# Kernel optimization log

Measured on AMD Instinct MI355X. Metric: run time of the kernel, lower is better.

The kernel has to match this reference:

```python
import jax, jax.numpy as jnp
import numpy as np
from jax import lax

EPS = 1e-05
Q = 4          # window size (hard-coded in BotBlock)
HEADS = 4
DIM = 16       # bottleneck(64) // heads(4)


def conv3x3(x, w, b):
    # x: [N,C,H,W], w: [O,I,3,3]
    y = lax.conv_general_dilated(x, w, (1, 1), ((1, 1), (1, 1)),
                                 dimension_numbers=('NCHW', 'OIHW', 'NCHW'))
    return y + b[None, :, None, None]


def batchnorm(x, gamma, beta):
    # training-mode BN: batch statistics over (N,H,W), biased variance
    m = jnp.mean(x, axis=(0, 2, 3), keepdims=True)
    v = jnp.var(x, axis=(0, 2, 3), keepdims=True)
    xn = (x - m) * lax.rsqrt(v + EPS)
    return xn * gamma[None, :, None, None] + beta[None, :, None, None]


def rel_to_abs(x):
    # x: [B, H, L, 2L-1] -> [B, H, L, L] via pad/reshape trick
    B, H, L, _ = x.shape
    x = jnp.pad(x, ((0, 0), (0, 0), (0, 0), (0, 1)))          # [B,H,L,2L]
    flat = x.reshape(B, H, -1)                                  # [B,H,2L*L]
    flat = jnp.pad(flat, ((0, 0), (0, 0), (0, L - 1)))
    final = flat.reshape(B, H, L + 1, 2 * L - 1)
    return final[:, :, :L, L - 1:]                              # [B,H,L,L]


def relative_logits_1d(q, rel_k, perm):
    # q: [b, n, h, w, d], rel_k: [2w-1, d]
    b, n, h, w, d = q.shape
    rl = jnp.einsum('bnhwd,md->bnhwm', q, rel_k)
    rl = rl.reshape(b, n * h, w, 2 * w - 1)
    rl = rel_to_abs(rl)                                         # [b, n*h, w, w]
    rl = rl.reshape(b, n, h, w, w)
    rl = jnp.broadcast_to(rl[:, :, :, None], (b, n, h, h, w, w))
    return jnp.transpose(rl, perm)


def rel_pos_attention(q, k, v, rel_w, rel_h):
    # q,k,v: [b, heads, h, w, d]
    b, n, h, w, d = q.shape
    q = q * (d ** -0.5)
    logits = jnp.einsum('bnhwd,bnpqd->bnhwpq', q, k)
    logits = logits + relative_logits_1d(q, rel_w, (0, 1, 2, 4, 3, 5))
    logits = logits + relative_logits_1d(jnp.transpose(q, (0, 1, 3, 2, 4)),
                                         rel_h, (0, 1, 4, 2, 5, 3))
    weights = jax.nn.softmax(logits.reshape(b, n, h, w, h * w), axis=-1)
    weights = weights.reshape(b, n, h, w, h, w)
    out = jnp.einsum('bnhwpq,bnpqd->bhwnd', weights, v)         # [b,h,w,n,d]
    return out.reshape(b, h, w, n * d)                          # fold heads


def setup_inputs() -> dict:
    key = jax.random.key(0)
    ks = jax.random.split(key, 16)
    C_in, C_bot, C_out = 64, 64, 256
    inp = {
        'x': jax.random.normal(ks[0], (2, C_in, 256, 256), jnp.float32),
        'conv1_w': jax.random.normal(ks[1], (C_bot, C_in, 3, 3), jnp.float32) * 0.05,
        'conv1_b': jnp.zeros((C_bot,), jnp.float32),
        'bn1_g': jnp.ones((C_bot,), jnp.float32),
        'bn1_b': jnp.zeros((C_bot,), jnp.float32),
        'wq': jax.random.normal(ks[2], (C_bot, HEADS, DIM), jnp.float32) * 0.01,
        'wk': jax.random.normal(ks[3], (C_bot, HEADS, DIM), jnp.float32) * 0.01,
        'wv': jax.random.normal(ks[4], (C_bot, HEADS, DIM), jnp.float32) * 0.01,
        'rel_w': jax.random.normal(ks[5], (2 * Q - 1, DIM), jnp.float32) * (DIM ** -0.5),
        'rel_h': jax.random.normal(ks[6], (2 * Q - 1, DIM), jnp.float32) * (DIM ** -0.5),
        'bn2_g': jnp.ones((C_bot,), jnp.float32),
        'bn2_b': jnp.zeros((C_bot,), jnp.float32),
        'conv3_w': jax.random.normal(ks[7], (C_out, C_bot, 3, 3), jnp.float32) * 0.05,
        'conv3_b': jnp.zeros((C_out,), jnp.float32),
        # NOTE: original init_zero=True zeros bn3 gamma; we randomize it so the
        # output (and gradients) are non-trivial for kernel correctness checks.
        'bn3_g': jax.random.normal(ks[8], (C_out,), jnp.float32),
        'bn3_b': jnp.zeros((C_out,), jnp.float32),
    }
    return inp


def reference(x, conv1_w, conv1_b, bn1_g, bn1_b, wq, wk, wv, rel_w, rel_h,
              bn2_g, bn2_b, conv3_w, conv3_b, bn3_g, bn3_b):
    N, C, H, W = x.shape
    P_h, P_w = H // Q, W // Q
    # raw memory reinterpretation into 4x4 blocks (matches torch .reshape)
    xb = x.reshape(N * P_h * P_w, C, Q, Q)
    out = jax.nn.relu(batchnorm(conv3x3(xb, conv1_w, conv1_b), bn1_g, bn1_b))
    # GroupPointWise projections: NCHW -> NHWC then einsum
    feat = jnp.transpose(out, (0, 2, 3, 1))                     # [b,h,w,c]
    q = jnp.einsum('bhwc,cnp->bnhwp', feat, wq)
    k = jnp.einsum('bhwc,cnp->bnhwp', feat, wk)
    v = jnp.einsum('bhwc,cnp->bnhwp', feat, wv)
    o = rel_pos_attention(q, k, v, rel_w, rel_h)                # [b,h,w,c]
    o = jnp.transpose(o, (0, 3, 1, 2))                          # NCHW
    o = jax.nn.relu(batchnorm(o, bn2_g, bn2_b))
    o = batchnorm(conv3x3(o, conv3_w, conv3_b), bn3_g, bn3_b)   # no act
    C1 = o.shape[1]
    o = o.reshape(N, C1, H, W)
    return jax.nn.relu(o)
```

## Files before the change

### kernel.cpp

```cpp
#include <hip/hip_runtime.h>
#include <stdint.h>


#define EPSV 1e-5f
#define INV_N (1.0f / 131072.0f)

typedef unsigned short u16;
typedef __attribute__((ext_vector_type(8))) short short8b;
typedef __attribute__((ext_vector_type(4))) float f32x4;

__device__ __forceinline__ u16 f2bf(float f) {
  unsigned u = __float_as_uint(f);
  u += 0x7fffu + ((u >> 16) & 1u);
  return (u16)(u >> 16);
}
__device__ __forceinline__ float bf2f(u16 h) {
  return __uint_as_float((unsigned)h << 16);
}

__device__ __forceinline__ float bn_scale(const float* __restrict__ acc,
                                          const float* __restrict__ gam,
                                          const float* __restrict__ bet,
                                          int C, int c, float& shift) {
  float S = acc[c], S2 = acc[C + c];
  float mean = S * INV_N;
  float var  = S2 * INV_N - mean * mean;
  float rstd = rsqrtf(var + EPSV);
  float sc = gam[c] * rstd;
  shift = bet[c] - mean * sc;
  return sc;
}

__global__ __launch_bounds__(256) void prep_kernel(const float* __restrict__ w1,
                                                   const float* __restrict__ w3,
                                                   const float* __restrict__ wq,
                                                   const float* __restrict__ wk,
                                                   const float* __restrict__ wv,
                                                   u16* __restrict__ wp1,
                                                   u16* __restrict__ wp3,
                                                   u16* __restrict__ wqkvT) {
  int i = blockIdx.x * 256 + threadIdx.x;
  const int tot1 = 18 * 64 * 40;
  const int tot3 = 9 * 256 * 64;
  if (i < tot1) {
    int ch = i / (64 * 40); int r = i - ch * 64 * 40; int o = r / 40; int kk = r - o * 40;
    float v = 0.f;
    if (kk < 32) { int k = ch * 32 + kk; int tap = k >> 6; int c = k & 63;
                   v = w1[o * 576 + c * 9 + tap]; }
    wp1[i] = f2bf(v);
  } else if (i < tot1 + tot3) {
    int j = i - tot1;
    int tap = j >> 14; int r = j & 16383; int o = r >> 6; int c = r & 63;
    wp3[j] = f2bf(w3[o * 576 + c * 9 + tap]);
  } else if (i < tot1 + tot3 + 192 * 64) {
    int j = i - tot1 - tot3;
    int oc = j >> 6, c = j & 63;
    const float* src = (oc < 64) ? wq : (oc < 128) ? wk : wv;
    wqkvT[j] = f2bf(src[(c << 6) + (oc & 63)]);
  }
}

__global__ __launch_bounds__(256) void conv1_kernel(const float* __restrict__ x,
                                                    const u16* __restrict__ wp,
                                                    u16* __restrict__ bufb,
                                                    float* __restrict__ partials1) {
  __shared__ __align__(16) char featA[257 * 128];
  __shared__ __align__(16) char ldsW[2][64 * 80];
  const int t = threadIdx.x;
  const int lane = t & 63, w = t >> 6;
  const int lrow = lane & 15, lk = lane >> 4;
  const int wm = w >> 1, wn = w & 1;
  const size_t Mbase = (size_t)blockIdx.x * 256;

  int rel[9];
  {
    const int pi = lrow >> 2, pj = lrow & 3;
#pragma unroll
    for (int tap = 0; tap < 9; ++tap) {
      const int ti = tap / 3, tj = tap - ti * 3;
      int si = pi + ti - 1, sj = pj + tj - 1;
      bool valid = ((unsigned)si < 4u) && ((unsigned)sj < 4u);
      rel[tap] = valid ? ((si * 4 + sj) << 7) : (1 << 24);
    }
  }

#pragma unroll
  for (int i = 0; i < 16; ++i) {
    float4 v = *reinterpret_cast<const float4*>(x + Mbase * 64 + i * 1024 + t * 4);
    const int c = t >> 2, p0 = (t & 3) * 4;
    float vv[4] = {v.x, v.y, v.z, v.w};
#pragma unroll
    for (int j = 0; j < 4; ++j) {
      int row = i * 16 + p0 + j;
      int byte = row * 128 + ((((c >> 3) ^ (row & 7)) << 4) | ((c & 7) << 1));
      *reinterpret_cast<u16*>(featA + byte) = f2bf(vv[j]);
    }
  }
  if (t < 8) *reinterpret_cast<uint4*>(featA + 256 * 128 + t * 16) = uint4{0, 0, 0, 0};

  uint4 s0, s1;
  {
    const u16* sp = wp;
    s0 = *reinterpret_cast<const uint4*>(sp + (size_t)t * 8);
    if (t < 64) s1 = *reinterpret_cast<const uint4*>(sp + (size_t)(t + 256) * 8);
    *reinterpret_cast<uint4*>(ldsW[0] + t * 16) = s0;
    if (t < 64) *reinterpret_cast<uint4*>(ldsW[0] + (t + 256) * 16) = s1;
  }
  __syncthreads();

  f32x4 acc[8][2] = {};
#pragma unroll
  for (int chn = 0; chn < 18; ++chn) {
    const int cur = chn & 1;
    const int tap = chn >> 1, kk = chn & 1;
    if (chn + 1 < 18) {
      const u16* sp = wp + (chn + 1) * 2560;
      s0 = *reinterpret_cast<const uint4*>(sp + (size_t)t * 8);
      if (t < 64) s1 = *reinterpret_cast<const uint4*>(sp + (size_t)(t + 256) * 8);
    }
    const int kkg = (kk << 6) | (lk << 4);
    short8b bw[2];
#pragma unroll
    for (int n = 0; n < 2; ++n)
      bw[n] = *reinterpret_cast<const short8b*>(ldsW[cur] + (wn * 32 + n * 16 + lrow) * 80 + lk * 16);
#pragma unroll
    for (int m = 0; m < 8; ++m) {
      int ad = ((wm * 128 + m * 16) << 7) + rel[tap];
      ad = ad < 32768 ? ad : 32768;
      ad += (kkg ^ ((ad >> 3) & 0x70));
      short8b af = *reinterpret_cast<const short8b*>(featA + ad);
#pragma unroll
      for (int n = 0; n < 2; ++n)
        acc[m][n] = __builtin_amdgcn_mfma_f32_16x16x32_bf16(af, bw[n], acc[m][n], 0, 0, 0);
    }
    if (chn + 1 < 18) {
      *reinterpret_cast<uint4*>(ldsW[cur ^ 1] + t * 16) = s0;
      if (t < 64) *reinterpret_cast<uint4*>(ldsW[cur ^ 1] + (t + 256) * 16) = s1;
    }
    __syncthreads();
  }

#pragma unroll
  for (int m = 0; m < 8; ++m) {
    const size_t rowg0 = Mbase + wm * 128 + m * 16 + lk * 4;
#pragma unroll
    for (int n = 0; n < 2; ++n) {
      const int o = wn * 32 + n * 16 + lrow;
#pragma unroll
      for (int r = 0; r < 4; ++r)
        bufb[(rowg0 + r) * 64 + o] = f2bf(acc[m][n][r]);
    }
  }

  float* pst = reinterpret_cast<float*>(featA);
  if (t < 128) pst[t] = 0.f;
  __syncthreads();
#pragma unroll
  for (int n = 0; n < 2; ++n) {
    float s = 0.f, s2 = 0.f;
#pragma unroll
    for (int m = 0; m < 8; ++m)
#pragma unroll
      for (int r = 0; r < 4; ++r) {
        float v = acc[m][n][r];
        s += v; s2 = fmaf(v, v, s2);
      }
    s += __shfl_xor(s, 16); s2 += __shfl_xor(s2, 16);
    s += __shfl_xor(s, 32); s2 += __shfl_xor(s2, 32);
    if (lk == 0) {
      const int o = wn * 32 + n * 16 + lrow;
      atomicAdd(&pst[o], s);
      atomicAdd(&pst[64 + o], s2);
    }
  }
  __syncthreads();
  if (t < 128) partials1[(size_t)blockIdx.x * 128 + t] = pst[t];
}

__global__ __launch_bounds__(256) void reduce12_kernel(const float* __restrict__ p,
                                                       float* __restrict__ acc, int nrows) {
  const int c = blockIdx.x, t = threadIdx.x;
  float s = 0.f;
  for (int i = t; i < nrows; i += 256) s += p[(size_t)i * 128 + c];
#pragma unroll
  for (int off = 32; off > 0; off >>= 1) s += __shfl_down(s, off);
  __shared__ float red[4];
  if ((t & 63) == 0) red[t >> 6] = s;
  __syncthreads();
  if (t == 0) acc[c] = red[0] + red[1] + red[2] + red[3];
}

__global__ __launch_bounds__(256) void attn_kernel(u16* __restrict__ buf,
                                                   const u16* __restrict__ wqkvT,
                                                   const float* __restrict__ relw,
                                                   const float* __restrict__ relh,
                                                   const float* __restrict__ acc1,
                                                   const float* __restrict__ g1,
                                                   const float* __restrict__ b1,
                                                   float* __restrict__ partials2) {
  __shared__ float scsh[64][2];
  __shared__ float pstA[128];
  __shared__ __align__(16) u16 feat_l[4][1024];
  __shared__ __align__(16) float qkvf[4][3264];
  const int t = threadIdx.x, u = t >> 6, lane = t & 63;
  const size_t b = (size_t)blockIdx.x * 4 + u;
  float* Wf = qkvf[u];

  if (t < 64) {
    float sh; float sc = bn_scale(acc1, g1, b1, 64, t, sh);
    scsh[t][0] = sc; scsh[t][1] = sh;
  }
  if (t < 128) pstA[t] = 0.f;
  __syncthreads();

  {
    const int pos = lane >> 2, cq = lane & 3;
    const u16* src = buf + b * 1024 + pos * 64 + cq * 16;
    short8b v0 = *reinterpret_cast<const short8b*>(src);
    short8b v1 = *reinterpret_cast<const short8b*>(src + 8);
    short8b p0, p1;
#pragma unroll
    for (int j = 0; j < 8; ++j) {
      const int c0 = cq * 16 + j, c1 = cq * 16 + 8 + j;
      p0[j] = (short)f2bf(fmaxf(fmaf(bf2f((u16)v0[j]), scsh[c0][0], scsh[c0][1]), 0.f));
      p1[j] = (short)f2bf(fmaxf(fmaf(bf2f((u16)v1[j]), scsh[c1][0], scsh[c1][1]), 0.f));
    }
    const int g0 = (cq * 2) ^ (pos & 7), g1g = (cq * 2 + 1) ^ (pos & 7);
    *reinterpret_cast<short8b*>(&feat_l[u][pos * 64 + g0 * 8]) = p0;
    *reinterpret_cast<short8b*>(&feat_l[u][pos * 64 + g1g * 8]) = p1;
  }

  const int dq = lane & 15, lk = lane >> 4;
  short8b afr[2];
#pragma unroll
  for (int ch = 0; ch < 2; ++ch) {
    const int kg = ch * 4 + lk;
    afr[ch] = *reinterpret_cast<const short8b*>(&feat_l[u][dq * 64 + ((kg ^ (dq & 7)) * 8)]);
  }
#pragma unroll
  for (int ct = 0; ct < 12; ++ct) {
    f32x4 d = {0.f, 0.f, 0.f, 0.f};
#pragma unroll
    for (int ch = 0; ch < 2; ++ch) {
      short8b bfr = *reinterpret_cast<const short8b*>(&wqkvT[(ct * 16 + dq) * 64 + ch * 32 + lk * 8]);
      d = __builtin_amdgcn_mfma_f32_16x16x32_bf16(afr[ch], bfr, d, 0, 0, 0);
    }
    if (ct < 4) {
      float* dst = Wf + ct * 280;
#pragma unroll
      for (int r = 0; r < 4; ++r) dst[(lk * 4 + r) * 17 + dq] = d[r] * 0.25f;
    } else {
      float* dst = (ct < 8) ? (Wf + 1120 + (ct - 4) * 264) : (Wf + 2176 + (ct - 8) * 264);
      const int cp = dq ^ (lk << 2);
#pragma unroll
      for (int r = 0; r < 4; ++r) dst[(lk * 4 + r) * 16 + cp] = d[r];
    }
  }

  const int n = lk, qp = dq;
  const int qi = qp >> 2, qj = qp & 3;
  float q_[16];
  {
    const float* qb = Wf + n * 280 + qp * 17;
#pragma unroll
    for (int d2 = 0; d2 < 16; ++d2) q_[d2] = qb[d2];
  }
  float rwq[4], rhq[4];
  {
    const float* rwp = relw + (3 - qj) * 16;
    const float* rhp = relh + (3 - qi) * 16;
#pragma unroll
    for (int m = 0; m < 4; ++m) {
      float a1 = 0.f, a2 = 0.f;
#pragma unroll
      for (int d2 = 0; d2 < 16; ++d2) {
        a1 = fmaf(q_[d2], rwp[m * 16 + d2], a1);
        a2 = fmaf(q_[d2], rhp[m * 16 + d2], a2);
      }
      rwq[m] = a1; rhq[m] = a2;
    }
  }
  float lo[16]; float mx = -1e30f;
  const float* kbase = Wf + 1120 + n * 264;
#pragma unroll
  for (int kp = 0; kp < 16; ++kp) {
    const float4* kr = reinterpret_cast<const float4*>(kbase + kp * 16);
    float s = rwq[kp & 3] + rhq[kp >> 2];
#pragma unroll
    for (int g = 0; g < 4; ++g) {
      float4 kv = kr[g];
      const int lg = (g ^ (kp >> 2)) * 4;
      s = fmaf(q_[lg], kv.x, s); s = fmaf(q_[lg + 1], kv.y, s);
      s = fmaf(q_[lg + 2], kv.z, s); s = fmaf(q_[lg + 3], kv.w, s);
    }
    lo[kp] = s; mx = fmaxf(mx, s);
  }
  float ssum = 0.f;
#pragma unroll
  for (int kp = 0; kp < 16; ++kp) { float e = __expf(lo[kp] - mx); lo[kp] = e; ssum += e; }
  const float inv = 1.0f / ssum;
  float ov[16];
#pragma unroll
  for (int j = 0; j < 16; ++j) ov[j] = 0.f;
  const float* vbase = Wf + 2176 + n * 264;
#pragma unroll
  for (int kp = 0; kp < 16; ++kp) {
    const float4* vr = reinterpret_cast<const float4*>(vbase + kp * 16);
    const float wgt = lo[kp];
#pragma unroll
    for (int g = 0; g < 4; ++g) {
      float4 vv = vr[g];
      const int lg = (g ^ (kp >> 2)) * 4;
      ov[lg] = fmaf(wgt, vv.x, ov[lg]);
      ov[lg + 1] = fmaf(wgt, vv.y, ov[lg + 1]);
      ov[lg + 2] = fmaf(wgt, vv.z, ov[lg + 2]);
      ov[lg + 3] = fmaf(wgt, vv.w, ov[lg + 3]);
    }
  }
#pragma unroll
  for (int j = 0; j < 16; ++j) ov[j] *= inv;

  {
    short8b o0, o1;
#pragma unroll
    for (int j = 0; j < 8; ++j) {
      o0[j] = (short)f2bf(ov[j]);
      o1[j] = (short)f2bf(ov[8 + j]);
    }
    u16* dstb = buf + b * 1024 + qp * 64 + (n << 4);
    *reinterpret_cast<short8b*>(dstb) = o0;
    *reinterpret_cast<short8b*>(dstb + 8) = o1;
  }

  {
    float* fl = Wf;
#pragma unroll
    for (int j = 0; j < 16; ++j) fl[qp * 69 + n * 16 + j] = ov[j];
    const int c = lane;
    float s = 0.f, s2 = 0.f;
#pragma unroll
    for (int pos = 0; pos < 16; ++pos) {
      float v = fl[pos * 69 + c];
      s += v; s2 = fmaf(v, v, s2);
    }
    atomicAdd(&pstA[c], s);
    atomicAdd(&pstA[64 + c], s2);
  }
  __syncthreads();
  if (t < 128) partials2[(size_t)blockIdx.x * 128 + t] = pstA[t];
}

__global__ __launch_bounds__(256, 2) void conv3_kernel(const u16* __restrict__ src,
                                                       const u16* __restrict__ wp,
                                                       const float* __restrict__ acc2,
                                                       const float* __restrict__ g2,
                                                       const float* __restrict__ b2,
                                                       u16* __restrict__ y3b,
                                                       float* __restrict__ partials3) {
  __shared__ __align__(16) u16 featB[257 * 64];
  __shared__ __align__(16) u16 ldsW[2][128 * 64];
  __shared__ float scsh[128];
  const int t = threadIdx.x;
  const int lane = t & 63, w = t >> 6;
  const int lrow = lane & 15, lk = lane >> 4;
  const int wm = w >> 1, wn = w & 1;
  const int Nbase = blockIdx.x * 256;
  const int ohalf = blockIdx.y;

  int rel[9];
  {
    const int pi = lrow >> 2, pj = lrow & 3;
#pragma unroll
    for (int tap = 0; tap < 9; ++tap) {
      const int ti = tap / 3, tj = tap - ti * 3;
      int si = pi + ti - 1, sj = pj + tj - 1;
      bool valid = ((unsigned)si < 4u) && ((unsigned)sj < 4u);
      rel[tap] = valid ? ((si * 4 + sj) << 7) : (1 << 24);
    }
  }

  if (t < 64) {
    float sh; float sc = bn_scale(acc2, g2, b2, 64, t, sh);
    scsh[t * 2] = sc; scsh[t * 2 + 1] = sh;
  }

  const int so = t >> 1, shalf = t & 1, so7 = so & 7;
  {
    const u16* wsrc = wp + ohalf * 8192 + so * 64 + shalf * 32;
    uint4 w0 = *reinterpret_cast<const uint4*>(wsrc);
    uint4 w1 = *reinterpret_cast<const uint4*>(wsrc + 8);
    uint4 w2 = *reinterpret_cast<const uint4*>(wsrc + 16);
    uint4 w3v = *reinterpret_cast<const uint4*>(wsrc + 24);
    char* dst = (char*)ldsW[0] + so * 128;
    const int gb = shalf * 4;
    *reinterpret_cast<uint4*>(dst + (((gb + 0) ^ so7) << 4)) = w0;
    *reinterpret_cast<uint4*>(dst + (((gb + 1) ^ so7) << 4)) = w1;
    *reinterpret_cast<uint4*>(dst + (((gb + 2) ^ so7) << 4)) = w2;
    *reinterpret_cast<uint4*>(dst + (((gb + 3) ^ so7) << 4)) = w3v;
  }
  __syncthreads();

  {
    const u16* srow = src + (size_t)(Nbase + t) * 64;
    char* drow = (char*)featB + t * 128;
    const int r7 = t & 7;
#pragma unroll
    for (int g = 0; g < 8; ++g) {
      short8b v = *reinterpret_cast<const short8b*>(srow + g * 8);
      short8b pk;
#pragma unroll
      for (int j = 0; j < 8; ++j) {
        const int c = g * 8 + j;
        pk[j] = (short)f2bf(fmaxf(fmaf(bf2f((u16)v[j]), scsh[c * 2], scsh[c * 2 + 1]), 0.f));
      }
      *reinterpret_cast<short8b*>(drow + ((g ^ r7) << 4)) = pk;
    }
  }
  if (t < 8) *reinterpret_cast<uint4*>((char*)featB + 32768 + t * 16) = uint4{0, 0, 0, 0};

  uint4 r0, r1, r2, r3v;
  {
    const u16* wsrc = wp + 16384 + ohalf * 8192 + so * 64 + shalf * 32;
    r0 = *reinterpret_cast<const uint4*>(wsrc);
    r1 = *reinterpret_cast<const uint4*>(wsrc + 8);
    r2 = *reinterpret_cast<const uint4*>(wsrc + 16);
    r3v = *reinterpret_cast<const uint4*>(wsrc + 24);
  }
  __syncthreads();

  f32x4 acc[4][8] = {};
  const char* fB = (const char*)featB;
  const int swzA0 = (lk << 4) ^ ((lrow & 7) << 4);
  const int swzA1 = (64 | (lk << 4)) ^ ((lrow & 7) << 4);

#pragma unroll
  for (int tap = 0; tap < 9; ++tap) {
    const int cur = tap & 1;
    const char* lW = (const char*)ldsW[cur];
    short8b aw0[4], aw1[4];
#pragma unroll
    for (int m = 0; m < 4; ++m) {
      const int rowoff = (wm * 64 + m * 16 + lrow) << 7;
      aw0[m] = *reinterpret_cast<const short8b*>(lW + rowoff + swzA0);
      aw1[m] = *reinterpret_cast<const short8b*>(lW + rowoff + swzA1);
    }
#pragma unroll
    for (int n = 0; n < 8; ++n) {
      int ad0 = ((wn * 128 + n * 16) << 7) + rel[tap];
      ad0 = ad0 < 32768 ? ad0 : 32768;
      const int swz = (ad0 >> 3) & 0x70;
      short8b bf0 = *reinterpret_cast<const short8b*>(fB + ad0 + ((lk << 4) ^ swz));
      short8b bf1 = *reinterpret_cast<const short8b*>(fB + ad0 + ((64 | (lk << 4)) ^ swz));
#pragma unroll
      for (int m = 0; m < 4; ++m) {
        acc[m][n] = __builtin_amdgcn_mfma_f32_16x16x32_bf16(aw0[m], bf0, acc[m][n], 0, 0, 0);
        acc[m][n] = __builtin_amdgcn_mfma_f32_16x16x32_bf16(aw1[m], bf1, acc[m][n], 0, 0, 0);
      }
    }
    if (tap < 8) {
      char* dst = (char*)ldsW[cur ^ 1] + so * 128;
      const int gb = shalf * 4;
      *reinterpret_cast<uint4*>(dst + (((gb + 0) ^ so7) << 4)) = r0;
      *reinterpret_cast<uint4*>(dst + (((gb + 1) ^ so7) << 4)) = r1;
      *reinterpret_cast<uint4*>(dst + (((gb + 2) ^ so7) << 4)) = r2;
      *reinterpret_cast<uint4*>(dst + (((gb + 3) ^ so7) << 4)) = r3v;
      if (tap < 7) {
        const u16* wsrc = wp + (tap + 2) * 16384 + ohalf * 8192 + so * 64 + shalf * 32;
        r0 = *reinterpret_cast<const uint4*>(wsrc);
        r1 = *reinterpret_cast<const uint4*>(wsrc + 8);
        r2 = *reinterpret_cast<const uint4*>(wsrc + 16);
        r3v = *reinterpret_cast<const uint4*>(wsrc + 24);
      }
    }
    __syncthreads();
  }

#pragma unroll
  for (int m = 0; m < 4; ++m) {
    const int o = ohalf * 128 + wm * 64 + m * 16 + lk * 4;
#pragma unroll
    for (int n = 0; n < 8; ++n) {
      const int colg = Nbase + wn * 128 + n * 16 + lrow;
      const int b = colg >> 4, p = colg & 15;
      u16* dst = y3b + (size_t)b * 4096 + (size_t)o * 16 + p;
#pragma unroll
      for (int r = 0; r < 4; ++r)
        dst[r * 16] = f2bf(acc[m][n][r]);
    }
  }

  float* pst = reinterpret_cast<float*>(featB);
  pst[t] = 0.f;
  __syncthreads();
#pragma unroll
  for (int m = 0; m < 4; ++m) {
#pragma unroll
    for (int r = 0; r < 4; ++r) {
      float s = 0.f, s2 = 0.f;
#pragma unroll
      for (int n = 0; n < 8; ++n) {
        float v = acc[m][n][r];
        s += v; s2 = fmaf(v, v, s2);
      }
      s += __shfl_xor(s, 1); s2 += __shfl_xor(s2, 1);
      s += __shfl_xor(s, 2); s2 += __shfl_xor(s2, 2);
      s += __shfl_xor(s, 4); s2 += __shfl_xor(s2, 4);
      s += __shfl_xor(s, 8); s2 += __shfl_xor(s2, 8);
      if (lrow == 0) {
        const int ch = wm * 64 + m * 16 + lk * 4 + r;
        atomicAdd(&pst[ch], s);
        atomicAdd(&pst[128 + ch], s2);
      }
    }
  }
  __syncthreads();
  partials3[((size_t)(ohalf * 512 + blockIdx.x)) * 256 + t] = pst[t];
}

__global__ __launch_bounds__(256) void reduce3_kernel(const float* __restrict__ p,
                                                      float* __restrict__ acc3) {
  const int c2 = blockIdx.x, t = threadIdx.x;
  const int kind = c2 >> 8, c = c2 & 255;
  const int h = c >> 7, chl = c & 127;
  float s = 0.f;
  for (int i = t; i < 512; i += 256)
    s += p[((size_t)(h * 512 + i)) * 256 + kind * 128 + chl];
#pragma unroll
  for (int off = 32; off > 0; off >>= 1) s += __shfl_down(s, off);
  __shared__ float red[4];
  if ((t & 63) == 0) red[t >> 6] = s;
  __syncthreads();
  if (t == 0) acc3[kind * 256 + c] = red[0] + red[1] + red[2] + red[3];
}

__global__ __launch_bounds__(256) void final_kernel(const u16* __restrict__ y3b,
                                                    float* __restrict__ out,
                                                    const float* __restrict__ acc3,
                                                    const float* __restrict__ g3,
                                                    const float* __restrict__ b3) {
  const size_t i = ((size_t)blockIdx.x * 256 + threadIdx.x) * 8;
  const int c = (int)((i >> 4) & 255);
  float sh; const float sc = bn_scale(acc3, g3, b3, 256, c, sh);
  short8b v = *reinterpret_cast<const short8b*>(y3b + i);
  float4 o0, o1;
  o0.x = fmaxf(fmaf(bf2f((u16)v[0]), sc, sh), 0.f);
  o0.y = fmaxf(fmaf(bf2f((u16)v[1]), sc, sh), 0.f);
  o0.z = fmaxf(fmaf(bf2f((u16)v[2]), sc, sh), 0.f);
  o0.w = fmaxf(fmaf(bf2f((u16)v[3]), sc, sh), 0.f);
  o1.x = fmaxf(fmaf(bf2f((u16)v[4]), sc, sh), 0.f);
  o1.y = fmaxf(fmaf(bf2f((u16)v[5]), sc, sh), 0.f);
  o1.z = fmaxf(fmaf(bf2f((u16)v[6]), sc, sh), 0.f);
  o1.w = fmaxf(fmaf(bf2f((u16)v[7]), sc, sh), 0.f);
  *reinterpret_cast<float4*>(out + i) = o0;
  *reinterpret_cast<float4*>(out + i + 4) = o1;
}

extern "C" void kernel_launch(void* const* d_in, const int* in_sizes, int n_in,
                              void* d_out, int out_size, void* d_ws, size_t ws_size,
                              hipStream_t stream) {
  const float* x   = (const float*)d_in[0];
  const float* w1  = (const float*)d_in[1];
  const float* g1  = (const float*)d_in[3];
  const float* bb1 = (const float*)d_in[4];
  const float* wq  = (const float*)d_in[5];
  const float* wk  = (const float*)d_in[6];
  const float* wv  = (const float*)d_in[7];
  const float* rw  = (const float*)d_in[8];
  const float* rh  = (const float*)d_in[9];
  const float* g2  = (const float*)d_in[10];
  const float* bb2 = (const float*)d_in[11];
  const float* w3  = (const float*)d_in[12];
  const float* g3  = (const float*)d_in[14];
  const float* bb3 = (const float*)d_in[15];
  float* out = (float*)d_out;
  float* ws  = (float*)d_ws;

  u16*   bufb   = (u16*)ws;
  u16*   y3b    = bufb + 8388608;
  u16*   wp1    = y3b + 33554432;
  u16*   wp3    = wp1 + 46080;
  u16*   wqkvT  = wp3 + 147456;
  float* acc1   = ws + 21074432;
  float* acc2   = acc1 + 128;
  float* acc3   = acc2 + 128;
  float* part1  = acc3 + 512;
  float* part2  = part1 + 65536;
  float* part3  = part2 + 262144;

  prep_kernel<<<804, 256, 0, stream>>>(w1, w3, wq, wk, wv, wp1, wp3, wqkvT);
  conv1_kernel<<<512, 256, 0, stream>>>(x, wp1, bufb, part1);
  reduce12_kernel<<<128, 256, 0, stream>>>(part1, acc1, 512);
  attn_kernel<<<2048, 256, 0, stream>>>(bufb, wqkvT, rw, rh, acc1, g1, bb1, part2);
  reduce12_kernel<<<128, 256, 0, stream>>>(part2, acc2, 2048);
  conv3_kernel<<<dim3(512, 2), 256, 0, stream>>>(bufb, wp3, acc2, g2, bb2, y3b, part3);
  reduce3_kernel<<<512, 256, 0, stream>>>(part3, acc3);
  final_kernel<<<16384, 256, 0, stream>>>(y3b, out, acc3, g3, bb3);
}
```

Measured before the change: 163.9 us.

## Fold relative-position logits into QKV MFMA and use packed bf16 conversions

```diff
diff --git a/kernel.cpp b/kernel.cpp
--- a/kernel.cpp
+++ b/kernel.cpp
@@ -16,6 +16,11 @@
 }
 __device__ __forceinline__ float bf2f(u16 h) {
   return __uint_as_float((unsigned)h << 16);
+}
+__device__ __forceinline__ unsigned cvtpk(float lo, float hi) {
+  unsigned r;
+  asm("v_cvt_pk_bf16_f32 %0, %1, %2" : "=v"(r) : "v"(lo), "v"(hi));
+  return r;
 }
 
 __device__ __forceinline__ float bn_scale(const float* __restrict__ acc,
@@ -36,6 +41,8 @@
                                                    const float* __restrict__ wq,
                                                    const float* __restrict__ wk,
                                                    const float* __restrict__ wv,
+                                                   const float* __restrict__ relw,
+                                                   const float* __restrict__ relh,
                                                    u16* __restrict__ wp1,
                                                    u16* __restrict__ wp3,
                                                    u16* __restrict__ wqkvT) {
@@ -57,6 +64,17 @@
     int oc = j >> 6, c = j & 63;
     const float* src = (oc < 64) ? wq : (oc < 128) ? wk : wv;
     wqkvT[j] = f2bf(src[(c << 6) + (oc & 63)]);
+  } else if (i < tot1 + tot3 + 192 * 64 + 4096) {
+    int j = i - tot1 - tot3 - 192 * 64;
+    int c = j & 63; int col = (j >> 6) & 31; int tbl = j >> 11;
+    int n = col >> 3, m = col & 7;
+    float v = 0.f;
+    if (m < 7) {
+      const float* rel = tbl ? relh : relw;
+#pragma unroll
+      for (int d = 0; d < 16; ++d) v += wq[c * 64 + n * 16 + d] * rel[m * 16 + d];
+    }
+    wqkvT[(192 + tbl * 32 + col) * 64 + c] = f2bf(v);
   }
 }
 
@@ -84,16 +102,21 @@
     }
   }
 
-#pragma unroll
-  for (int i = 0; i < 16; ++i) {
-    float4 v = *reinterpret_cast<const float4*>(x + Mbase * 64 + i * 1024 + t * 4);
-    const int c = t >> 2, p0 = (t & 3) * 4;
-    float vv[4] = {v.x, v.y, v.z, v.w};
-#pragma unroll
-    for (int j = 0; j < 4; ++j) {
-      int row = i * 16 + p0 + j;
-      int byte = row * 128 + ((((c >> 3) ^ (row & 7)) << 4) | ((c & 7) << 1));
-      *reinterpret_cast<u16*>(featA + byte) = f2bf(vv[j]);
+  {
+    const int cp = t >> 3, ph = t & 7;
+    const int gsw = ((cp >> 2) << 4) | ((cp & 3) << 2);
+#pragma unroll
+    for (int i = 0; i < 16; ++i) {
+      const float* bp = x + Mbase * 64 + i * 1024 + cp * 32 + ph * 2;
+      float2 a = *reinterpret_cast<const float2*>(bp);
+      float2 b = *reinterpret_cast<const float2*>(bp + 16);
+#pragma unroll
+      for (int j = 0; j < 2; ++j) {
+        const int row = i * 16 + ph * 2 + j;
+        unsigned pk = cvtpk(j ? a.y : a.x, j ? b.y : b.x);
+        const int byte = row * 128 + (gsw ^ ((row & 7) << 4));
+        *reinterpret_cast<unsigned*>(featA + byte) = pk;
+      }
     }
   }
   if (t < 8) *reinterpret_cast<uint4*>(featA + 256 * 128 + t * 16) = uint4{0, 0, 0, 0};
@@ -192,8 +215,6 @@
 
 __global__ __launch_bounds__(256) void attn_kernel(u16* __restrict__ buf,
                                                    const u16* __restrict__ wqkvT,
-                                                   const float* __restrict__ relw,
-                                                   const float* __restrict__ relh,
                                                    const float* __restrict__ acc1,
                                                    const float* __restrict__ g1,
                                                    const float* __restrict__ b1,
@@ -201,10 +222,12 @@
   __shared__ float scsh[64][2];
   __shared__ float pstA[128];
   __shared__ __align__(16) u16 feat_l[4][1024];
-  __shared__ __align__(16) float qkvf[4][3264];
+  __shared__ __align__(16) float qkvf[4][3200];
+  __shared__ __align__(16) float relLs[4][1152];
   const int t = threadIdx.x, u = t >> 6, lane = t & 63;
   const size_t b = (size_t)blockIdx.x * 4 + u;
   float* Wf = qkvf[u];
+  float* rL = relLs[u];
 
   if (t < 64) {
     float sh; float sc = bn_scale(acc1, g1, b1, 64, t, sh);
@@ -218,16 +241,18 @@
     const u16* src = buf + b * 1024 + pos * 64 + cq * 16;
     short8b v0 = *reinterpret_cast<const short8b*>(src);
     short8b v1 = *reinterpret_cast<const short8b*>(src + 8);
-    short8b p0, p1;
+    float f[16];
 #pragma unroll
     for (int j = 0; j < 8; ++j) {
       const int c0 = cq * 16 + j, c1 = cq * 16 + 8 + j;
-      p0[j] = (short)f2bf(fmaxf(fmaf(bf2f((u16)v0[j]), scsh[c0][0], scsh[c0][1]), 0.f));
-      p1[j] = (short)f2bf(fmaxf(fmaf(bf2f((u16)v1[j]), scsh[c1][0], scsh[c1][1]), 0.f));
-    }
+      f[j]     = fmaxf(fmaf(bf2f((u16)v0[j]), scsh[c0][0], scsh[c0][1]), 0.f);
+      f[8 + j] = fmaxf(fmaf(bf2f((u16)v1[j]), scsh[c1][0], scsh[c1][1]), 0.f);
+    }
+    uint4 q0{cvtpk(f[0], f[1]), cvtpk(f[2], f[3]), cvtpk(f[4], f[5]), cvtpk(f[6], f[7])};
+    uint4 q1{cvtpk(f[8], f[9]), cvtpk(f[10], f[11]), cvtpk(f[12], f[13]), cvtpk(f[14], f[15])};
     const int g0 = (cq * 2) ^ (pos & 7), g1g = (cq * 2 + 1) ^ (pos & 7);
-    *reinterpret_cast<short8b*>(&feat_l[u][pos * 64 + g0 * 8]) = p0;
-    *reinterpret_cast<short8b*>(&feat_l[u][pos * 64 + g1g * 8]) = p1;
+    *reinterpret_cast<uint4*>(&feat_l[u][pos * 64 + g0 * 8]) = q0;
+    *reinterpret_cast<uint4*>(&feat_l[u][pos * 64 + g1g * 8]) = q1;
   }
 
   const int dq = lane & 15, lk = lane >> 4;
@@ -238,7 +263,7 @@
     afr[ch] = *reinterpret_cast<const short8b*>(&feat_l[u][dq * 64 + ((kg ^ (dq & 7)) * 8)]);
   }
 #pragma unroll
-  for (int ct = 0; ct < 12; ++ct) {
+  for (int ct = 0; ct < 16; ++ct) {
     f32x4 d = {0.f, 0.f, 0.f, 0.f};
 #pragma unroll
     for (int ch = 0; ch < 2; ++ch) {
@@ -246,14 +271,20 @@
       d = __builtin_amdgcn_mfma_f32_16x16x32_bf16(afr[ch], bfr, d, 0, 0, 0);
     }
     if (ct < 4) {
-      float* dst = Wf + ct * 280;
+      float* dst = Wf + ct * 272;
 #pragma unroll
       for (int r = 0; r < 4; ++r) dst[(lk * 4 + r) * 17 + dq] = d[r] * 0.25f;
+    } else if (ct < 12) {
+      float* dst = (ct < 8) ? (Wf + 1088 + (ct - 4) * 264) : (Wf + 2144 + (ct - 8) * 264);
+      const int cp = dq ^ (lk << 2);
+#pragma unroll
+      for (int r = 0; r < 4; ++r) dst[(lk * 4 + r) * 16 + cp] = d[r];
     } else {
-      float* dst = (ct < 8) ? (Wf + 1120 + (ct - 4) * 264) : (Wf + 2176 + (ct - 8) * 264);
-      const int cp = dq ^ (lk << 2);
-#pragma unroll
-      for (int r = 0; r < 4; ++r) dst[(lk * 4 + r) * 16 + cp] = d[r];
+      const int rc = ct - 12, tbl = rc >> 1;
+      const int nn = ((rc & 1) << 1) | (dq >> 3), mm = dq & 7;
+      float* dst = rL + tbl * 576 + nn * 144 + mm;
+#pragma unroll
+      for (int r = 0; r < 4; ++r) dst[(lk * 4 + r) * 9] = d[r] * 0.25f;
     }
   }
 
@@ -261,27 +292,19 @@
   const int qi = qp >> 2, qj = qp & 3;
   float q_[16];
   {
-    const float* qb = Wf + n * 280 + qp * 17;
+    const float* qb = Wf + n * 272 + qp * 17;
 #pragma unroll
     for (int d2 = 0; d2 < 16; ++d2) q_[d2] = qb[d2];
   }
   float rwq[4], rhq[4];
   {
-    const float* rwp = relw + (3 - qj) * 16;
-    const float* rhp = relh + (3 - qi) * 16;
-#pragma unroll
-    for (int m = 0; m < 4; ++m) {
-      float a1 = 0.f, a2 = 0.f;
-#pragma unroll
-      for (int d2 = 0; d2 < 16; ++d2) {
-        a1 = fmaf(q_[d2], rwp[m * 16 + d2], a1);
-        a2 = fmaf(q_[d2], rhp[m * 16 + d2], a2);
-      }
-      rwq[m] = a1; rhq[m] = a2;
-    }
+    const float* rw = rL + n * 144 + qp * 9 + (3 - qj);
+    const float* rh = rL + 576 + n * 144 + qp * 9 + (3 - qi);
+#pragma unroll
+    for (int k = 0; k < 4; ++k) { rwq[k] = rw[k]; rhq[k] = rh[k]; }
   }
   float lo[16]; float mx = -1e30f;
-  const float* kbase = Wf + 1120 + n * 264;
+  const float* kbase = Wf + 1088 + n * 264;
 #pragma unroll
   for (int kp = 0; kp < 16; ++kp) {
     const float4* kr = reinterpret_cast<const float4*>(kbase + kp * 16);
@@ -302,7 +325,7 @@
   float ov[16];
 #pragma unroll
   for (int j = 0; j < 16; ++j) ov[j] = 0.f;
-  const float* vbase = Wf + 2176 + n * 264;
+  const float* vbase = Wf + 2144 + n * 264;
 #pragma unroll
   for (int kp = 0; kp < 16; ++kp) {
     const float4* vr = reinterpret_cast<const float4*>(vbase + kp * 16);
@@ -321,15 +344,11 @@
   for (int j = 0; j < 16; ++j) ov[j] *= inv;
 
   {
-    short8b o0, o1;
-#pragma unroll
-    for (int j = 0; j < 8; ++j) {
-      o0[j] = (short)f2bf(ov[j]);
-      o1[j] = (short)f2bf(ov[8 + j]);
-    }
+    uint4 o0{cvtpk(ov[0], ov[1]), cvtpk(ov[2], ov[3]), cvtpk(ov[4], ov[5]), cvtpk(ov[6], ov[7])};
+    uint4 o1{cvtpk(ov[8], ov[9]), cvtpk(ov[10], ov[11]), cvtpk(ov[12], ov[13]), cvtpk(ov[14], ov[15])};
     u16* dstb = buf + b * 1024 + qp * 64 + (n << 4);
-    *reinterpret_cast<short8b*>(dstb) = o0;
-    *reinterpret_cast<short8b*>(dstb + 8) = o1;
+    *reinterpret_cast<uint4*>(dstb) = o0;
+    *reinterpret_cast<uint4*>(dstb + 8) = o1;
   }
 
   {
@@ -378,12 +397,10 @@
       rel[tap] = valid ? ((si * 4 + sj) << 7) : (1 << 24);
     }
   }
-
   if (t < 64) {
     float sh; float sc = bn_scale(acc2, g2, b2, 64, t, sh);
     scsh[t * 2] = sc; scsh[t * 2 + 1] = sh;
   }
-
   const int so = t >> 1, shalf = t & 1, so7 = so & 7;
   {
     const u16* wsrc = wp + ohalf * 8192 + so * 64 + shalf * 32;
@@ -399,7 +416,6 @@
     *reinterpret_cast<uint4*>(dst + (((gb + 3) ^ so7) << 4)) = w3v;
   }
   __syncthreads();
-
   {
     const u16* srow = src + (size_t)(Nbase + t) * 64;
     char* drow = (char*)featB + t * 128;
@@ -407,17 +423,17 @@
 #pragma unroll
     for (int g = 0; g < 8; ++g) {
       short8b v = *reinterpret_cast<const short8b*>(srow + g * 8);
-      short8b pk;
+      float f[8];
 #pragma unroll
       for (int j = 0; j < 8; ++j) {
         const int c = g * 8 + j;
-        pk[j] = (short)f2bf(fmaxf(fmaf(bf2f((u16)v[j]), scsh[c * 2], scsh[c * 2 + 1]), 0.f));
+        f[j] = fmaxf(fmaf(bf2f((u16)v[j]), scsh[c * 2], scsh[c * 2 + 1]), 0.f);
       }
-      *reinterpret_cast<short8b*>(drow + ((g ^ r7) << 4)) = pk;
+      uint4 pk{cvtpk(f[0], f[1]), cvtpk(f[2], f[3]), cvtpk(f[4], f[5]), cvtpk(f[6], f[7])};
+      *reinterpret_cast<uint4*>(drow + ((g ^ r7) << 4)) = pk;
     }
   }
   if (t < 8) *reinterpret_cast<uint4*>((char*)featB + 32768 + t * 16) = uint4{0, 0, 0, 0};
-
   uint4 r0, r1, r2, r3v;
   {
     const u16* wsrc = wp + 16384 + ohalf * 8192 + so * 64 + shalf * 32;
@@ -427,12 +443,10 @@
     r3v = *reinterpret_cast<const uint4*>(wsrc + 24);
   }
   __syncthreads();
-
   f32x4 acc[4][8] = {};
   const char* fB = (const char*)featB;
   const int swzA0 = (lk << 4) ^ ((lrow & 7) << 4);
   const int swzA1 = (64 | (lk << 4)) ^ ((lrow & 7) << 4);
-
 #pragma unroll
   for (int tap = 0; tap < 9; ++tap) {
     const int cur = tap & 1;
@@ -474,7 +488,6 @@
     }
     __syncthreads();
   }
-
 #pragma unroll
   for (int m = 0; m < 4; ++m) {
     const int o = ohalf * 128 + wm * 64 + m * 16 + lk * 4;
@@ -484,11 +497,9 @@
       const int b = colg >> 4, p = colg & 15;
       u16* dst = y3b + (size_t)b * 4096 + (size_t)o * 16 + p;
 #pragma unroll
-      for (int r = 0; r < 4; ++r)
-        dst[r * 16] = f2bf(acc[m][n][r]);
-    }
-  }
-
+      for (int r = 0; r < 4; ++r) dst[r * 16] = f2bf(acc[m][n][r]);
+    }
+  }
   float* pst = reinterpret_cast<float*>(featB);
   pst[t] = 0.f;
   __syncthreads();
@@ -576,23 +587,23 @@
   float* ws  = (float*)d_ws;
 
   u16*   bufb   = (u16*)ws;
-  u16*   y3b    = bufb + 8388608;
-  u16*   wp1    = y3b + 33554432;
+  u16*   y3     = bufb + 8388608;
+  u16*   wp1    = y3 + 33554432;
   u16*   wp3    = wp1 + 46080;
   u16*   wqkvT  = wp3 + 147456;
-  float* acc1   = ws + 21074432;
+  float* acc1   = ws + 21076480;
   float* acc2   = acc1 + 128;
   float* acc3   = acc2 + 128;
   float* part1  = acc3 + 512;
   float* part2  = part1 + 65536;
   float* part3  = part2 + 262144;
 
-  prep_kernel<<<804, 256, 0, stream>>>(w1, w3, wq, wk, wv, wp1, wp3, wqkvT);
+  prep_kernel<<<820, 256, 0, stream>>>(w1, w3, wq, wk, wv, rw, rh, wp1, wp3, wqkvT);
   conv1_kernel<<<512, 256, 0, stream>>>(x, wp1, bufb, part1);
   reduce12_kernel<<<128, 256, 0, stream>>>(part1, acc1, 512);
-  attn_kernel<<<2048, 256, 0, stream>>>(bufb, wqkvT, rw, rh, acc1, g1, bb1, part2);
+  attn_kernel<<<2048, 256, 0, stream>>>(bufb, wqkvT, acc1, g1, bb1, part2);
   reduce12_kernel<<<128, 256, 0, stream>>>(part2, acc2, 2048);
-  conv3_kernel<<<dim3(512, 2), 256, 0, stream>>>(bufb, wp3, acc2, g2, bb2, y3b, part3);
+  conv3_kernel<<<dim3(512, 2), 256, 0, stream>>>(bufb, wp3, acc2, g2, bb2, y3, part3);
   reduce3_kernel<<<512, 256, 0, stream>>>(part3, acc3);
-  final_kernel<<<16384, 256, 0, stream>>>(y3b, out, acc3, g3, bb3);
-}
+  final_kernel<<<16384, 256, 0, stream>>>(y3, out, acc3, g3, bb3);
+}
```

Result: faster. 159.9 us (-2.4%).
